# Performance work log

Measured on AMD Instinct MI355X. Metric: run time of the kernel, lower is better.

Reference implementation:

```python
import jax, jax.numpy as jnp
from jax import lax
import numpy as np

BETA = 0.9
SLOPE = 25.0  # snntorch fast_sigmoid default slope

@jax.custom_vjp
def spike_fn(mem_shift):
    # Heaviside forward, fast-sigmoid surrogate backward
    return (mem_shift > 0).astype(mem_shift.dtype)

def _spike_fwd(mem_shift):
    return spike_fn(mem_shift), mem_shift

def _spike_bwd(mem_shift, g):
    return (g / (SLOPE * jnp.abs(mem_shift) + 1.0) ** 2,)

spike_fn.defvjp(_spike_fwd, _spike_bwd)

def lif_step(inp, mem, thr):
    # snntorch Leaky, reset_mechanism='subtract': reset computed from PREVIOUS mem, detached
    reset = lax.stop_gradient((mem - thr > 0).astype(mem.dtype))
    mem_new = BETA * mem + inp - reset * thr  # thr keeps grad through reset term
    spk = spike_fn(mem_new - thr)
    return spk, mem_new

def _linear_init(key, out_f, in_f):
    k1, k2 = jax.random.split(key)
    bound = 1.0 / np.sqrt(in_f)
    W = jax.random.uniform(k1, (out_f, in_f), jnp.float32, -bound, bound)
    b = jax.random.uniform(k2, (out_f,), jnp.float32, -bound, bound)
    return W, b

def setup_inputs() -> dict:
    key = jax.random.key(0)
    ks = jax.random.split(key, 6)
    B, T = 2048, 112
    x = jax.random.normal(ks[0], (B, T, 4), jnp.float32)
    W1, b1 = _linear_init(ks[1], 1300, 4)
    W2, b2 = _linear_init(ks[2], 340, 1300)
    W3, b3 = _linear_init(ks[3], 1400, 340)
    W4, b4 = _linear_init(ks[4], 4, 1400)
    return {
        'x': x,
        'W1': W1, 'b1': b1, 'bias1': jnp.zeros((1300,), jnp.float32),
        'W2': W2, 'b2': b2, 'bias2': jnp.zeros((340,), jnp.float32),
        'W3': W3, 'b3': b3, 'bias3': jnp.zeros((1400,), jnp.float32),
        'W4': W4, 'b4': b4, 'bias4': jnp.zeros((4,), jnp.float32),
        'thr4': jnp.asarray(0.5, jnp.float32),
    }

def reference(x, W1, b1, bias1, W2, b2, bias2, W3, b3, bias3, W4, b4, bias4, thr4):
    B, T, _ = x.shape
    one = jnp.asarray(1.0, x.dtype)

    def step(carry, xt):
        m1, m2, m3, m4 = carry
        xt = xt / 50.0 + 0.001
        s1, m1 = lif_step(xt @ W1.T + b1 + bias1, m1, one)
        s2, m2 = lif_step(s1 @ W2.T + b2 + bias2, m2, one)
        s3, m3 = lif_step(s2 @ W3.T + b3 + bias3, m3, one)
        s4, m4 = lif_step(s3 @ W4.T + b4 + bias4, m4, thr4)
        return (m1, m2, m3, m4), s4

    init = tuple(jnp.zeros((B, d), x.dtype) for d in (1300, 340, 1400, 4))
    _, spk4 = lax.scan(step, init, jnp.swapaxes(x, 0, 1))  # [T,B,4]
    spk4_stack = jnp.swapaxes(spk4, 0, 1)  # [B,T,4]
    spike_counts = spk4_stack.sum(axis=1)  # [B,4]
    return spike_counts, spk4_stack
```

## Files before the change

kernel.cpp:

```cpp
#include <hip/hip_runtime.h>

#define B_ROWS  2048
#define T_STEPS 112
#define N1 1300
#define N2 340
#define N3 1400

#define R1 384
#define R2 128
#define R3 384

#define OFF_W2T 0
#define OFF_W3T 442000
#define OFF_W4T 918000
#define OFF_BS1 923600
#define OFF_BS2 924900
#define OFF_BS3 925240
#define OFF_BS4 926640
#define WS_FLOATS 926644

__global__ __launch_bounds__(256) void snn_prep(
    const float* __restrict__ W2, const float* __restrict__ W3, const float* __restrict__ W4,
    const float* __restrict__ b1, const float* __restrict__ bias1,
    const float* __restrict__ b2, const float* __restrict__ bias2,
    const float* __restrict__ b3, const float* __restrict__ bias3,
    const float* __restrict__ b4, const float* __restrict__ bias4,
    float* __restrict__ ws)
{
    for (int idx = blockIdx.x * blockDim.x + threadIdx.x; idx < WS_FLOATS;
         idx += gridDim.x * blockDim.x) {
        float v;
        if (idx < OFF_W3T) {
            int j = idx; int i = j / N2, k = j % N2;
            v = W2[k * N1 + i];
        } else if (idx < OFF_W4T) {
            int j = idx - OFF_W3T; int i = j / N3, k = j % N3;
            v = W3[k * N2 + i];
        } else if (idx < OFF_BS1) {
            int j = idx - OFF_W4T; int i = j / 4, k = j % 4;
            v = W4[k * N3 + i];
        } else if (idx < OFF_BS2) { int j = idx - OFF_BS1; v = b1[j] + bias1[j]; }
        else if (idx < OFF_BS3)   { int j = idx - OFF_BS2; v = b2[j] + bias2[j]; }
        else if (idx < OFF_BS4)   { int j = idx - OFF_BS3; v = b3[j] + bias3[j]; }
        else                      { int j = idx - OFF_BS4; v = b4[j] + bias4[j]; }
        ws[idx] = v;
    }
}

__global__ __launch_bounds__(256, 3) void snn_main(
    const float* __restrict__ x,
    const float* __restrict__ W1,
    const float* __restrict__ ws,
    const float* __restrict__ thr4p,
    float* __restrict__ out)
{
    const int b    = blockIdx.x;
    const int tid  = threadIdx.x;
    const int wave = tid >> 6;
    const int lane = tid & 63;

    const float* __restrict__ W2T = ws + OFF_W2T;
    const float* __restrict__ W3T = ws + OFF_W3T;
    const float* __restrict__ W4T = ws + OFF_W4T;
    const float* __restrict__ bs1 = ws + OFF_BS1;
    const float* __restrict__ bs2 = ws + OFF_BS2;
    const float* __restrict__ bs3 = ws + OFF_BS3;
    const float* __restrict__ bs4 = ws + OFF_BS4;

    __shared__ __align__(16) float pw2[4][340];
    __shared__ __align__(16) float pw3[4][1400];
    __shared__ __align__(16) unsigned lst1[4 * R1];
    __shared__ __align__(16) unsigned lst2[4 * R2];
    __shared__ __align__(16) unsigned lst3[4 * R3];
    __shared__ int wcnt3[4];
    __shared__ float sbuf[T_STEPS * 4];

    const int c1b = (wave == 0) ? 0 : (wave == 1) ? 6 : (wave == 2) ? 11 : 16;
    const int n1  = (wave == 0) ? 6 : 5;

    float mem1[6] = {0.f,0.f,0.f,0.f,0.f,0.f};
    float mem2[2] = {0.f,0.f};
    float mem3[6] = {0.f,0.f,0.f,0.f,0.f,0.f};
    float mem4 = 0.f;
    float cnt  = 0.f;
    const float thr4 = thr4p[0];

    const float4* __restrict__ xv4 = (const float4*)x;
    const float4* __restrict__ W1v = (const float4*)W1;

    int  k1v[6]; bool val1[6]; float bsv1[6];
    #pragma unroll
    for (int u = 0; u < 6; ++u) {
        k1v[u] = (c1b + u) * 64 + lane;
        val1[u] = (u < n1) && (k1v[u] < N1);
        bsv1[u] = val1[u] ? bs1[k1v[u]] : 0.f;
    }
    const bool  has2  = (tid < 84);
    const float bs2v0 = bs2[tid];
    const float bs2v1 = has2 ? bs2[tid + 256] : 0.f;
    float bs3v[6];
    #pragma unroll
    for (int k = 0; k < 5; ++k) bs3v[k] = bs3[tid + 256 * k];
    bs3v[5] = (tid < 120) ? bs3[tid + 1280] : 0.f;
    const float bs4v = bs4[lane & 3];

    const int   so2    = (lane < 21) ? 4 * lane : 80;
    const float mask21 = (lane < 21) ? 1.f : 0.f;
    const int   so3    = (lane < 30) ? 4 * lane : 116;
    const float mask30 = (lane < 30) ? 1.f : 0.f;

    for (int t = 0; t < T_STEPS; ++t) {
        float4 xv = xv4[b * T_STEPS + t];
        const float x0 = xv.x / 50.0f + 0.001f;
        const float x1 = xv.y / 50.0f + 0.001f;
        const float x2 = xv.z / 50.0f + 0.001f;
        const float x3 = xv.w / 50.0f + 0.001f;

        unsigned cnt1w = 0;
        #pragma unroll
        for (int u = 0; u < 6; ++u) {
            if (u < n1) {
                float h = 0.f;
                if (val1[u]) {
                    float4 wv = W1v[k1v[u]];
                    h = bsv1[u] + wv.x * x0 + wv.y * x1 + wv.z * x2 + wv.w * x3;
                }
                float m = mem1[u];
                const float r = (m > 1.0f) ? 1.0f : 0.0f;
                m = 0.9f * m + h - r;
                mem1[u] = m;
                const bool sp = val1[u] && (m > 1.0f);
                const unsigned long long bal = __ballot(sp);
                if (sp) {
                    const int pos = (int)cnt1w + (int)__popcll(bal & ((1ull << lane) - 1ull));
                    lst1[wave * R1 + pos] = (unsigned)(k1v[u] * N2);
                }
                cnt1w += (unsigned)__popcll(bal);
            }
        }

        float4 accA = {0.f,0.f,0.f,0.f};
        float4 accB = {0.f,0.f,0.f,0.f};
        {
            const unsigned* L1w  = lst1 + wave * R1;
            const float* baseA = W2T + 4 * lane;
            const float* baseB = W2T + 256 + so2;
            int j = 0;
            for (; j + 4 <= (int)cnt1w; j += 4) {
                uint4 ov = *(const uint4*)(L1w + j);
                float4 r0 = *(const float4*)(baseA + ov.x);
                float4 r1 = *(const float4*)(baseA + ov.y);
                float4 r2 = *(const float4*)(baseA + ov.z);
                float4 r3 = *(const float4*)(baseA + ov.w);
                float4 s0 = *(const float4*)(baseB + ov.x);
                float4 s1 = *(const float4*)(baseB + ov.y);
                float4 s2 = *(const float4*)(baseB + ov.z);
                float4 s3 = *(const float4*)(baseB + ov.w);
                accA.x += r0.x; accA.y += r0.y; accA.z += r0.z; accA.w += r0.w;
                accB.x += s0.x * mask21; accB.y += s0.y * mask21; accB.z += s0.z * mask21; accB.w += s0.w * mask21;
                accA.x += r1.x; accA.y += r1.y; accA.z += r1.z; accA.w += r1.w;
                accB.x += s1.x * mask21; accB.y += s1.y * mask21; accB.z += s1.z * mask21; accB.w += s1.w * mask21;
                accA.x += r2.x; accA.y += r2.y; accA.z += r2.z; accA.w += r2.w;
                accB.x += s2.x * mask21; accB.y += s2.y * mask21; accB.z += s2.z * mask21; accB.w += s2.w * mask21;
                accA.x += r3.x; accA.y += r3.y; accA.z += r3.z; accA.w += r3.w;
                accB.x += s3.x * mask21; accB.y += s3.y * mask21; accB.z += s3.z * mask21; accB.w += s3.w * mask21;
            }
            for (; j < (int)cnt1w; ++j) {
                const unsigned o = L1w[j];
                float4 r = *(const float4*)(baseA + o);
                float4 s = *(const float4*)(baseB + o);
                accA.x += r.x; accA.y += r.y; accA.z += r.z; accA.w += r.w;
                accB.x += s.x * mask21; accB.y += s.y * mask21; accB.z += s.z * mask21; accB.w += s.w * mask21;
            }
        }
        *(float4*)&pw2[wave][4 * lane] = accA;
        if (lane < 21) *(float4*)&pw2[wave][256 + 4 * lane] = accB;
        __syncthreads();

        unsigned cnt2w = 0;
        {
            const float h0 = pw2[0][tid] + pw2[1][tid] + pw2[2][tid] + pw2[3][tid] + bs2v0;
            float m = mem2[0];
            const float r = (m > 1.0f) ? 1.0f : 0.0f;
            m = 0.9f * m + h0 - r;
            mem2[0] = m;
            const bool sp0 = (m > 1.0f);
            const unsigned long long bal0 = __ballot(sp0);
            if (sp0) {
                const int pos = (int)__popcll(bal0 & ((1ull << lane) - 1ull));
                lst2[wave * R2 + pos] = (unsigned)(tid * N3);
            }
            cnt2w += (unsigned)__popcll(bal0);

            float h1 = 0.f;
            if (has2) h1 = pw2[0][tid+256] + pw2[1][tid+256] + pw2[2][tid+256] + pw2[3][tid+256] + bs2v1;
            float m1v = mem2[1];
            const float r1v = (m1v > 1.0f) ? 1.0f : 0.0f;
            m1v = 0.9f * m1v + h1 - r1v;
            mem2[1] = m1v;
            const bool sp1 = has2 && (m1v > 1.0f);
            const unsigned long long bal1 = __ballot(sp1);
            if (sp1) {
                const int pos = (int)cnt2w + (int)__popcll(bal1 & ((1ull << lane) - 1ull));
                lst2[wave * R2 + pos] = (unsigned)((tid + 256) * N3);
            }
            cnt2w += (unsigned)__popcll(bal1);
        }

        float4 acc3[6];
        #pragma unroll
        for (int c = 0; c < 6; ++c) acc3[c] = (float4){0.f,0.f,0.f,0.f};
        {
            const unsigned* L2w = lst2 + wave * R2;
            int j = 0;
            for (; j + 2 <= (int)cnt2w; j += 2) {
                uint2 ov = *(const uint2*)(L2w + j);
                const float* ra = W3T + ov.x;
                const float* rb = W3T + ov.y;
                float4 a0 = *(const float4*)(ra + 4*lane);
                float4 a1 = *(const float4*)(ra + 256 + 4*lane);
                float4 a2 = *(const float4*)(ra + 512 + 4*lane);
                float4 a3 = *(const float4*)(ra + 768 + 4*lane);
                float4 a4 = *(const float4*)(ra + 1024 + 4*lane);
                float4 a5 = *(const float4*)(ra + 1280 + so3);
                float4 b0 = *(const float4*)(rb + 4*lane);
                float4 b1_ = *(const float4*)(rb + 256 + 4*lane);
                float4 b2_ = *(const float4*)(rb + 512 + 4*lane);
                float4 b3_ = *(const float4*)(rb + 768 + 4*lane);
                float4 b4_ = *(const float4*)(rb + 1024 + 4*lane);
                float4 b5_ = *(const float4*)(rb + 1280 + so3);
                acc3[0].x += a0.x; acc3[0].y += a0.y; acc3[0].z += a0.z; acc3[0].w += a0.w;
                acc3[1].x += a1.x; acc3[1].y += a1.y; acc3[1].z += a1.z; acc3[1].w += a1.w;
                acc3[2].x += a2.x; acc3[2].y += a2.y; acc3[2].z += a2.z; acc3[2].w += a2.w;
                acc3[3].x += a3.x; acc3[3].y += a3.y; acc3[3].z += a3.z; acc3[3].w += a3.w;
                acc3[4].x += a4.x; acc3[4].y += a4.y; acc3[4].z += a4.z; acc3[4].w += a4.w;
                acc3[5].x += a5.x * mask30; acc3[5].y += a5.y * mask30; acc3[5].z += a5.z * mask30; acc3[5].w += a5.w * mask30;
                acc3[0].x += b0.x; acc3[0].y += b0.y; acc3[0].z += b0.z; acc3[0].w += b0.w;
                acc3[1].x += b1_.x; acc3[1].y += b1_.y; acc3[1].z += b1_.z; acc3[1].w += b1_.w;
                acc3[2].x += b2_.x; acc3[2].y += b2_.y; acc3[2].z += b2_.z; acc3[2].w += b2_.w;
                acc3[3].x += b3_.x; acc3[3].y += b3_.y; acc3[3].z += b3_.z; acc3[3].w += b3_.w;
                acc3[4].x += b4_.x; acc3[4].y += b4_.y; acc3[4].z += b4_.z; acc3[4].w += b4_.w;
                acc3[5].x += b5_.x * mask30; acc3[5].y += b5_.y * mask30; acc3[5].z += b5_.z * mask30; acc3[5].w += b5_.w * mask30;
            }
            for (; j < (int)cnt2w; ++j) {
                const float* ra = W3T + L2w[j];
                float4 a0 = *(const float4*)(ra + 4*lane);
                float4 a1 = *(const float4*)(ra + 256 + 4*lane);
                float4 a2 = *(const float4*)(ra + 512 + 4*lane);
                float4 a3 = *(const float4*)(ra + 768 + 4*lane);
                float4 a4 = *(const float4*)(ra + 1024 + 4*lane);
                float4 a5 = *(const float4*)(ra + 1280 + so3);
                acc3[0].x += a0.x; acc3[0].y += a0.y; acc3[0].z += a0.z; acc3[0].w += a0.w;
                acc3[1].x += a1.x; acc3[1].y += a1.y; acc3[1].z += a1.z; acc3[1].w += a1.w;
                acc3[2].x += a2.x; acc3[2].y += a2.y; acc3[2].z += a2.z; acc3[2].w += a2.w;
                acc3[3].x += a3.x; acc3[3].y += a3.y; acc3[3].z += a3.z; acc3[3].w += a3.w;
                acc3[4].x += a4.x; acc3[4].y += a4.y; acc3[4].z += a4.z; acc3[4].w += a4.w;
                acc3[5].x += a5.x * mask30; acc3[5].y += a5.y * mask30; acc3[5].z += a5.z * mask30; acc3[5].w += a5.w * mask30;
            }
        }
        #pragma unroll
        for (int c = 0; c < 5; ++c)
            *(float4*)&pw3[wave][c * 256 + 4 * lane] = acc3[c];
        if (lane < 30) *(float4*)&pw3[wave][1280 + 4 * lane] = acc3[5];
        __syncthreads();

        unsigned cnt3w = 0;
        #pragma unroll
        for (int k = 0; k < 6; ++k) {
            const bool valid = (k < 5) || (tid < 120);
            const int n = tid + 256 * k;
            float h = 0.f;
            if (valid) h = pw3[0][n] + pw3[1][n] + pw3[2][n] + pw3[3][n] + bs3v[k];
            float m = mem3[k];
            const float r = (m > 1.0f) ? 1.0f : 0.0f;
            m = 0.9f * m + h - r;
            mem3[k] = m;
            const bool sp = valid && (m > 1.0f);
            const unsigned long long bal = __ballot(sp);
            if (sp) {
                const int pos = (int)cnt3w + (int)__popcll(bal & ((1ull << lane) - 1ull));
                lst3[wave * R3 + pos] = (unsigned)(n * 4);
            }
            cnt3w += (unsigned)__popcll(bal);
        }
        if (lane == 0) wcnt3[wave] = (int)cnt3w;
        __syncthreads();

        if (wave == 3) {
            const int g16 = lane >> 2;
            const int o4  = lane & 3;
            float h4p = 0.f;
            for (int w = 0; w < 4; ++w) {
                const int n = wcnt3[w];
                const unsigned* Lw = lst3 + w * R3;
                int j = g16;
                for (; j + 48 < n; j += 64) {
                    float t0 = W4T[Lw[j]      + o4];
                    float t1 = W4T[Lw[j + 16] + o4];
                    float t2 = W4T[Lw[j + 32] + o4];
                    float t3 = W4T[Lw[j + 48] + o4];
                    h4p += t0; h4p += t1; h4p += t2; h4p += t3;
                }
                for (; j < n; j += 16) h4p += W4T[Lw[j] + o4];
            }
            #pragma unroll
            for (int d = 4; d < 64; d <<= 1) h4p += __shfl_xor(h4p, d);
            float h4 = bs4v + h4p;
            float m4 = mem4;
            const float r4 = (m4 > thr4) ? thr4 : 0.f;
            m4 = 0.9f * m4 + h4 - r4;
            mem4 = m4;
            const float s4 = (m4 > thr4) ? 1.f : 0.f;
            if (lane < 4) {
                sbuf[t * 4 + lane] = s4;
                cnt += s4;
            }
        }
    }

    __syncthreads();
    for (int i = threadIdx.x; i < T_STEPS * 4; i += 256)
        out[8192 + b * T_STEPS * 4 + i] = sbuf[i];
    if (wave == 3 && lane < 4) out[b * 4 + lane] = cnt;
}

extern "C" void kernel_launch(void* const* d_in, const int* in_sizes, int n_in,
                              void* d_out, int out_size, void* d_ws, size_t ws_size,
                              hipStream_t stream)
{
    const float* x     = (const float*)d_in[0];
    const float* W1    = (const float*)d_in[1];
    const float* b1    = (const float*)d_in[2];
    const float* bias1 = (const float*)d_in[3];
    const float* W2    = (const float*)d_in[4];
    const float* b2    = (const float*)d_in[5];
    const float* bias2 = (const float*)d_in[6];
    const float* W3    = (const float*)d_in[7];
    const float* b3    = (const float*)d_in[8];
    const float* bias3 = (const float*)d_in[9];
    const float* W4    = (const float*)d_in[10];
    const float* b4    = (const float*)d_in[11];
    const float* bias4 = (const float*)d_in[12];
    const float* thr4  = (const float*)d_in[13];
    float* out = (float*)d_out;
    float* ws  = (float*)d_ws;

    hipLaunchKernelGGL(snn_prep, dim3(1024), dim3(256), 0, stream,
                       W2, W3, W4, b1, bias1, b2, bias2, b3, bias3, b4, bias4, ws);
    hipLaunchKernelGGL(snn_main, dim3(B_ROWS), dim3(256), 0, stream,
                       x, W1, ws, thr4, out);
}
```

Before: 2.199 ms.

## Drop a per-step barrier, compress spike lists to 16-bit, raise occupancy

Each wave now reduces its own layer-3 spike list against W4T and writes per-wave partials to shared memory. Layer-4 membrane integration is deferred to the next timestep, after an existing barrier, which removes one __syncthreads per step and the serial wave-3 gather. Spike index lists shrink from 32-bit offsets to 16-bit neuron indices, with the row multiply done at use, and R2 shrinks. Together these cut LDS use so launch bounds can request 4 blocks per CU. The layer-2 gather is unrolled to 8, and the per-element mask multiplies are dropped because masked lanes are never stored.

```diff
diff --git a/kernel.cpp b/kernel.cpp
--- a/kernel.cpp
+++ b/kernel.cpp
@@ -7,7 +7,7 @@
 #define N3 1400
 
 #define R1 384
-#define R2 128
+#define R2 96
 #define R3 384
 
 #define OFF_W2T 0
@@ -47,7 +47,7 @@
     }
 }
 
-__global__ __launch_bounds__(256, 3) void snn_main(
+__global__ __launch_bounds__(256, 4) void snn_main(
     const float* __restrict__ x,
     const float* __restrict__ W1,
     const float* __restrict__ ws,
@@ -69,11 +69,10 @@
 
     __shared__ __align__(16) float pw2[4][340];
     __shared__ __align__(16) float pw3[4][1400];
-    __shared__ __align__(16) unsigned lst1[4 * R1];
-    __shared__ __align__(16) unsigned lst2[4 * R2];
-    __shared__ __align__(16) unsigned lst3[4 * R3];
-    __shared__ int wcnt3[4];
-    __shared__ float sbuf[T_STEPS * 4];
+    __shared__ __align__(16) unsigned short lst1[4 * R1];
+    __shared__ __align__(16) unsigned short lst2[4 * R2];
+    __shared__ __align__(16) unsigned short lst3[4 * R3];
+    __shared__ float h4part[4][4];
 
     const int c1b = (wave == 0) ? 0 : (wave == 1) ? 6 : (wave == 2) ? 11 : 16;
     const int n1  = (wave == 0) ? 6 : 5;
@@ -104,10 +103,8 @@
     bs3v[5] = (tid < 120) ? bs3[tid + 1280] : 0.f;
     const float bs4v = bs4[lane & 3];
 
-    const int   so2    = (lane < 21) ? 4 * lane : 80;
-    const float mask21 = (lane < 21) ? 1.f : 0.f;
-    const int   so3    = (lane < 30) ? 4 * lane : 116;
-    const float mask30 = (lane < 30) ? 1.f : 0.f;
+    const int so2 = (lane < 21) ? 4 * lane : 80;
+    const int so3 = (lane < 30) ? 4 * lane : 116;
 
     for (int t = 0; t < T_STEPS; ++t) {
         float4 xv = xv4[b * T_STEPS + t];
@@ -133,49 +130,107 @@
                 const unsigned long long bal = __ballot(sp);
                 if (sp) {
                     const int pos = (int)cnt1w + (int)__popcll(bal & ((1ull << lane) - 1ull));
-                    lst1[wave * R1 + pos] = (unsigned)(k1v[u] * N2);
+                    lst1[wave * R1 + pos] = (unsigned short)k1v[u];
                 }
                 cnt1w += (unsigned)__popcll(bal);
             }
         }
 
-        float4 accA = {0.f,0.f,0.f,0.f};
-        float4 accB = {0.f,0.f,0.f,0.f};
         {
-            const unsigned* L1w  = lst1 + wave * R1;
+            float4 accA = {0.f,0.f,0.f,0.f};
+            float4 accB = {0.f,0.f,0.f,0.f};
+            const unsigned short* L = lst1 + wave * R1;
             const float* baseA = W2T + 4 * lane;
             const float* baseB = W2T + 256 + so2;
             int j = 0;
+            for (; j + 8 <= (int)cnt1w; j += 8) {
+                ushort4 i0 = *(const ushort4*)(L + j);
+                ushort4 i1 = *(const ushort4*)(L + j + 4);
+                const int o0 = (int)i0.x * N2, o1 = (int)i0.y * N2;
+                const int o2 = (int)i0.z * N2, o3 = (int)i0.w * N2;
+                const int o4 = (int)i1.x * N2, o5 = (int)i1.y * N2;
+                const int o6 = (int)i1.z * N2, o7 = (int)i1.w * N2;
+                float4 rA0 = *(const float4*)(baseA + o0);
+                float4 rA1 = *(const float4*)(baseA + o1);
+                float4 rA2 = *(const float4*)(baseA + o2);
+                float4 rA3 = *(const float4*)(baseA + o3);
+                float4 rA4 = *(const float4*)(baseA + o4);
+                float4 rA5 = *(const float4*)(baseA + o5);
+                float4 rA6 = *(const float4*)(baseA + o6);
+                float4 rA7 = *(const float4*)(baseA + o7);
+                float4 rB0 = *(const float4*)(baseB + o0);
+                float4 rB1 = *(const float4*)(baseB + o1);
+                float4 rB2 = *(const float4*)(baseB + o2);
+                float4 rB3 = *(const float4*)(baseB + o3);
+                float4 rB4 = *(const float4*)(baseB + o4);
+                float4 rB5 = *(const float4*)(baseB + o5);
+                float4 rB6 = *(const float4*)(baseB + o6);
+                float4 rB7 = *(const float4*)(baseB + o7);
+                accA.x += rA0.x; accA.y += rA0.y; accA.z += rA0.z; accA.w += rA0.w;
+                accB.x += rB0.x; accB.y += rB0.y; accB.z += rB0.z; accB.w += rB0.w;
+                accA.x += rA1.x; accA.y += rA1.y; accA.z += rA1.z; accA.w += rA1.w;
+                accB.x += rB1.x; accB.y += rB1.y; accB.z += rB1.z; accB.w += rB1.w;
+                accA.x += rA2.x; accA.y += rA2.y; accA.z += rA2.z; accA.w += rA2.w;
+                accB.x += rB2.x; accB.y += rB2.y; accB.z += rB2.z; accB.w += rB2.w;
+                accA.x += rA3.x; accA.y += rA3.y; accA.z += rA3.z; accA.w += rA3.w;
+                accB.x += rB3.x; accB.y += rB3.y; accB.z += rB3.z; accB.w += rB3.w;
+                accA.x += rA4.x; accA.y += rA4.y; accA.z += rA4.z; accA.w += rA4.w;
+                accB.x += rB4.x; accB.y += rB4.y; accB.z += rB4.z; accB.w += rB4.w;
+                accA.x += rA5.x; accA.y += rA5.y; accA.z += rA5.z; accA.w += rA5.w;
+                accB.x += rB5.x; accB.y += rB5.y; accB.z += rB5.z; accB.w += rB5.w;
+                accA.x += rA6.x; accA.y += rA6.y; accA.z += rA6.z; accA.w += rA6.w;
+                accB.x += rB6.x; accB.y += rB6.y; accB.z += rB6.z; accB.w += rB6.w;
+                accA.x += rA7.x; accA.y += rA7.y; accA.z += rA7.z; accA.w += rA7.w;
+                accB.x += rB7.x; accB.y += rB7.y; accB.z += rB7.z; accB.w += rB7.w;
+            }
             for (; j + 4 <= (int)cnt1w; j += 4) {
-                uint4 ov = *(const uint4*)(L1w + j);
-                float4 r0 = *(const float4*)(baseA + ov.x);
-                float4 r1 = *(const float4*)(baseA + ov.y);
-                float4 r2 = *(const float4*)(baseA + ov.z);
-                float4 r3 = *(const float4*)(baseA + ov.w);
-                float4 s0 = *(const float4*)(baseB + ov.x);
-                float4 s1 = *(const float4*)(baseB + ov.y);
-                float4 s2 = *(const float4*)(baseB + ov.z);
-                float4 s3 = *(const float4*)(baseB + ov.w);
-                accA.x += r0.x; accA.y += r0.y; accA.z += r0.z; accA.w += r0.w;
-                accB.x += s0.x * mask21; accB.y += s0.y * mask21; accB.z += s0.z * mask21; accB.w += s0.w * mask21;
-                accA.x += r1.x; accA.y += r1.y; accA.z += r1.z; accA.w += r1.w;
-                accB.x += s1.x * mask21; accB.y += s1.y * mask21; accB.z += s1.z * mask21; accB.w += s1.w * mask21;
-                accA.x += r2.x; accA.y += r2.y; accA.z += r2.z; accA.w += r2.w;
-                accB.x += s2.x * mask21; accB.y += s2.y * mask21; accB.z += s2.z * mask21; accB.w += s2.w * mask21;
-                accA.x += r3.x; accA.y += r3.y; accA.z += r3.z; accA.w += r3.w;
-                accB.x += s3.x * mask21; accB.y += s3.y * mask21; accB.z += s3.z * mask21; accB.w += s3.w * mask21;
+                ushort4 i0 = *(const ushort4*)(L + j);
+                const int o0 = (int)i0.x * N2, o1 = (int)i0.y * N2;
+                const int o2 = (int)i0.z * N2, o3 = (int)i0.w * N2;
+                float4 rA0 = *(const float4*)(baseA + o0);
+                float4 rA1 = *(const float4*)(baseA + o1);
+                float4 rA2 = *(const float4*)(baseA + o2);
+                float4 rA3 = *(const float4*)(baseA + o3);
+                float4 rB0 = *(const float4*)(baseB + o0);
+                float4 rB1 = *(const float4*)(baseB + o1);
+                float4 rB2 = *(const float4*)(baseB + o2);
+                float4 rB3 = *(const float4*)(baseB + o3);
+                accA.x += rA0.x; accA.y += rA0.y; accA.z += rA0.z; accA.w += rA0.w;
+                accB.x += rB0.x; accB.y += rB0.y; accB.z += rB0.z; accB.w += rB0.w;
+                accA.x += rA1.x; accA.y += rA1.y; accA.z += rA1.z; accA.w += rA1.w;
+                accB.x += rB1.x; accB.y += rB1.y; accB.z += rB1.z; accB.w += rB1.w;
+                accA.x += rA2.x; accA.y += rA2.y; accA.z += rA2.z; accA.w += rA2.w;
+                accB.x += rB2.x; accB.y += rB2.y; accB.z += rB2.z; accB.w += rB2.w;
+                accA.x += rA3.x; accA.y += rA3.y; accA.z += rA3.z; accA.w += rA3.w;
+                accB.x += rB3.x; accB.y += rB3.y; accB.z += rB3.z; accB.w += rB3.w;
             }
             for (; j < (int)cnt1w; ++j) {
-                const unsigned o = L1w[j];
-                float4 r = *(const float4*)(baseA + o);
-                float4 s = *(const float4*)(baseB + o);
-                accA.x += r.x; accA.y += r.y; accA.z += r.z; accA.w += r.w;
-                accB.x += s.x * mask21; accB.y += s.y * mask21; accB.z += s.z * mask21; accB.w += s.w * mask21;
-            }
-        }
-        *(float4*)&pw2[wave][4 * lane] = accA;
-        if (lane < 21) *(float4*)&pw2[wave][256 + 4 * lane] = accB;
+                const int o = (int)L[j] * N2;
+                float4 rA = *(const float4*)(baseA + o);
+                float4 rB = *(const float4*)(baseB + o);
+                accA.x += rA.x; accA.y += rA.y; accA.z += rA.z; accA.w += rA.w;
+                accB.x += rB.x; accB.y += rB.y; accB.z += rB.z; accB.w += rB.w;
+            }
+            *(float4*)&pw2[wave][4 * lane] = accA;
+            if (lane < 21) *(float4*)&pw2[wave][256 + 4 * lane] = accB;
+        }
         __syncthreads();
+
+        if (wave == 3 && t > 0) {
+            float h4 = bs4v + h4part[0][lane & 3];
+            h4 += h4part[1][lane & 3];
+            h4 += h4part[2][lane & 3];
+            h4 += h4part[3][lane & 3];
+            float m4 = mem4;
+            const float r4 = (m4 > thr4) ? thr4 : 0.f;
+            m4 = 0.9f * m4 + h4 - r4;
+            mem4 = m4;
+            const float s4 = (m4 > thr4) ? 1.f : 0.f;
+            if (lane < 4) {
+                out[8192 + (b * T_STEPS + (t - 1)) * 4 + lane] = s4;
+                cnt += s4;
+            }
+        }
 
         unsigned cnt2w = 0;
         {
@@ -188,7 +243,7 @@
             const unsigned long long bal0 = __ballot(sp0);
             if (sp0) {
                 const int pos = (int)__popcll(bal0 & ((1ull << lane) - 1ull));
-                lst2[wave * R2 + pos] = (unsigned)(tid * N3);
+                lst2[wave * R2 + pos] = (unsigned short)tid;
             }
             cnt2w += (unsigned)__popcll(bal0);
 
@@ -202,21 +257,21 @@
             const unsigned long long bal1 = __ballot(sp1);
             if (sp1) {
                 const int pos = (int)cnt2w + (int)__popcll(bal1 & ((1ull << lane) - 1ull));
-                lst2[wave * R2 + pos] = (unsigned)((tid + 256) * N3);
+                lst2[wave * R2 + pos] = (unsigned short)(tid + 256);
             }
             cnt2w += (unsigned)__popcll(bal1);
         }
 
-        float4 acc3[6];
-        #pragma unroll
-        for (int c = 0; c < 6; ++c) acc3[c] = (float4){0.f,0.f,0.f,0.f};
         {
-            const unsigned* L2w = lst2 + wave * R2;
+            float4 acc3[6];
+            #pragma unroll
+            for (int c = 0; c < 6; ++c) acc3[c] = (float4){0.f,0.f,0.f,0.f};
+            const unsigned short* L = lst2 + wave * R2;
             int j = 0;
             for (; j + 2 <= (int)cnt2w; j += 2) {
-                uint2 ov = *(const uint2*)(L2w + j);
-                const float* ra = W3T + ov.x;
-                const float* rb = W3T + ov.y;
+                ushort2 ii = *(const ushort2*)(L + j);
+                const float* ra = W3T + (int)ii.x * N3;
+                const float* rb = W3T + (int)ii.y * N3;
                 float4 a0 = *(const float4*)(ra + 4*lane);
                 float4 a1 = *(const float4*)(ra + 256 + 4*lane);
                 float4 a2 = *(const float4*)(ra + 512 + 4*lane);
@@ -234,16 +289,16 @@
                 acc3[2].x += a2.x; acc3[2].y += a2.y; acc3[2].z += a2.z; acc3[2].w += a2.w;
                 acc3[3].x += a3.x; acc3[3].y += a3.y; acc3[3].z += a3.z; acc3[3].w += a3.w;
                 acc3[4].x += a4.x; acc3[4].y += a4.y; acc3[4].z += a4.z; acc3[4].w += a4.w;
-                acc3[5].x += a5.x * mask30; acc3[5].y += a5.y * mask30; acc3[5].z += a5.z * mask30; acc3[5].w += a5.w * mask30;
+                acc3[5].x += a5.x; acc3[5].y += a5.y; acc3[5].z += a5.z; acc3[5].w += a5.w;
                 acc3[0].x += b0.x; acc3[0].y += b0.y; acc3[0].z += b0.z; acc3[0].w += b0.w;
                 acc3[1].x += b1_.x; acc3[1].y += b1_.y; acc3[1].z += b1_.z; acc3[1].w += b1_.w;
                 acc3[2].x += b2_.x; acc3[2].y += b2_.y; acc3[2].z += b2_.z; acc3[2].w += b2_.w;
                 acc3[3].x += b3_.x; acc3[3].y += b3_.y; acc3[3].z += b3_.z; acc3[3].w += b3_.w;
                 acc3[4].x += b4_.x; acc3[4].y += b4_.y; acc3[4].z += b4_.z; acc3[4].w += b4_.w;
-                acc3[5].x += b5_.x * mask30; acc3[5].y += b5_.y * mask30; acc3[5].z += b5_.z * mask30; acc3[5].w += b5_.w * mask30;
+                acc3[5].x += b5_.x; acc3[5].y += b5_.y; acc3[5].z += b5_.z; acc3[5].w += b5_.w;
             }
             for (; j < (int)cnt2w; ++j) {
-                const float* ra = W3T + L2w[j];
+                const float* ra = W3T + (int)L[j] * N3;
                 float4 a0 = *(const float4*)(ra + 4*lane);
                 float4 a1 = *(const float4*)(ra + 256 + 4*lane);
                 float4 a2 = *(const float4*)(ra + 512 + 4*lane);
@@ -255,73 +310,68 @@
                 acc3[2].x += a2.x; acc3[2].y += a2.y; acc3[2].z += a2.z; acc3[2].w += a2.w;
                 acc3[3].x += a3.x; acc3[3].y += a3.y; acc3[3].z += a3.z; acc3[3].w += a3.w;
                 acc3[4].x += a4.x; acc3[4].y += a4.y; acc3[4].z += a4.z; acc3[4].w += a4.w;
-                acc3[5].x += a5.x * mask30; acc3[5].y += a5.y * mask30; acc3[5].z += a5.z * mask30; acc3[5].w += a5.w * mask30;
-            }
-        }
-        #pragma unroll
-        for (int c = 0; c < 5; ++c)
-            *(float4*)&pw3[wave][c * 256 + 4 * lane] = acc3[c];
-        if (lane < 30) *(float4*)&pw3[wave][1280 + 4 * lane] = acc3[5];
+                acc3[5].x += a5.x; acc3[5].y += a5.y; acc3[5].z += a5.z; acc3[5].w += a5.w;
+            }
+            #pragma unroll
+            for (int c = 0; c < 5; ++c)
+                *(float4*)&pw3[wave][c * 256 + 4 * lane] = acc3[c];
+            if (lane < 30) *(float4*)&pw3[wave][1280 + 4 * lane] = acc3[5];
+        }
         __syncthreads();
 
-        unsigned cnt3w = 0;
-        #pragma unroll
-        for (int k = 0; k < 6; ++k) {
-            const bool valid = (k < 5) || (tid < 120);
-            const int n = tid + 256 * k;
-            float h = 0.f;
-            if (valid) h = pw3[0][n] + pw3[1][n] + pw3[2][n] + pw3[3][n] + bs3v[k];
-            float m = mem3[k];
-            const float r = (m > 1.0f) ? 1.0f : 0.0f;
-            m = 0.9f * m + h - r;
-            mem3[k] = m;
-            const bool sp = valid && (m > 1.0f);
-            const unsigned long long bal = __ballot(sp);
-            if (sp) {
-                const int pos = (int)cnt3w + (int)__popcll(bal & ((1ull << lane) - 1ull));
-                lst3[wave * R3 + pos] = (unsigned)(n * 4);
-            }
-            cnt3w += (unsigned)__popcll(bal);
-        }
-        if (lane == 0) wcnt3[wave] = (int)cnt3w;
-        __syncthreads();
-
-        if (wave == 3) {
-            const int g16 = lane >> 2;
-            const int o4  = lane & 3;
+        {
+            unsigned cnt3w = 0;
+            #pragma unroll
+            for (int k = 0; k < 6; ++k) {
+                const bool valid = (k < 5) || (tid < 120);
+                const int n = tid + 256 * k;
+                float h = 0.f;
+                if (valid) h = pw3[0][n] + pw3[1][n] + pw3[2][n] + pw3[3][n] + bs3v[k];
+                float m = mem3[k];
+                const float r = (m > 1.0f) ? 1.0f : 0.0f;
+                m = 0.9f * m + h - r;
+                mem3[k] = m;
+                const bool sp = valid && (m > 1.0f);
+                const unsigned long long bal = __ballot(sp);
+                if (sp) {
+                    const int pos = (int)cnt3w + (int)__popcll(bal & ((1ull << lane) - 1ull));
+                    lst3[wave * R3 + pos] = (unsigned short)n;
+                }
+                cnt3w += (unsigned)__popcll(bal);
+            }
             float h4p = 0.f;
-            for (int w = 0; w < 4; ++w) {
-                const int n = wcnt3[w];
-                const unsigned* Lw = lst3 + w * R3;
-                int j = g16;
-                for (; j + 48 < n; j += 64) {
-                    float t0 = W4T[Lw[j]      + o4];
-                    float t1 = W4T[Lw[j + 16] + o4];
-                    float t2 = W4T[Lw[j + 32] + o4];
-                    float t3 = W4T[Lw[j + 48] + o4];
-                    h4p += t0; h4p += t1; h4p += t2; h4p += t3;
-                }
-                for (; j < n; j += 16) h4p += W4T[Lw[j] + o4];
-            }
-            #pragma unroll
-            for (int d = 4; d < 64; d <<= 1) h4p += __shfl_xor(h4p, d);
-            float h4 = bs4v + h4p;
-            float m4 = mem4;
-            const float r4 = (m4 > thr4) ? thr4 : 0.f;
-            m4 = 0.9f * m4 + h4 - r4;
-            mem4 = m4;
-            const float s4 = (m4 > thr4) ? 1.f : 0.f;
-            if (lane < 4) {
-                sbuf[t * 4 + lane] = s4;
-                cnt += s4;
-            }
+            const unsigned short* L = lst3 + wave * R3;
+            const int o4 = lane & 3;
+            int j = 0;
+            for (; j + 4 <= (int)cnt3w; j += 4) {
+                ushort4 ii = *(const ushort4*)(L + j);
+                float t0 = W4T[4 * (int)ii.x + o4];
+                float t1 = W4T[4 * (int)ii.y + o4];
+                float t2 = W4T[4 * (int)ii.z + o4];
+                float t3 = W4T[4 * (int)ii.w + o4];
+                h4p += t0; h4p += t1; h4p += t2; h4p += t3;
+            }
+            for (; j < (int)cnt3w; ++j) h4p += W4T[4 * (int)L[j] + o4];
+            if (lane < 4) h4part[wave][lane] = h4p;
         }
     }
 
     __syncthreads();
-    for (int i = threadIdx.x; i < T_STEPS * 4; i += 256)
-        out[8192 + b * T_STEPS * 4 + i] = sbuf[i];
-    if (wave == 3 && lane < 4) out[b * 4 + lane] = cnt;
+    if (wave == 3) {
+        float h4 = bs4v + h4part[0][lane & 3];
+        h4 += h4part[1][lane & 3];
+        h4 += h4part[2][lane & 3];
+        h4 += h4part[3][lane & 3];
+        float m4 = mem4;
+        const float r4 = (m4 > thr4) ? thr4 : 0.f;
+        m4 = 0.9f * m4 + h4 - r4;
+        const float s4 = (m4 > thr4) ? 1.f : 0.f;
+        if (lane < 4) {
+            out[8192 + (b * T_STEPS + (T_STEPS - 1)) * 4 + lane] = s4;
+            cnt += s4;
+            out[b * 4 + lane] = cnt;
+        }
+    }
 }
 
 extern "C" void kernel_launch(void* const* d_in, const int* in_sizes, int n_in,
```

New measurement: 2.689 ms. 22.3% more time.
